# Kernel optimization log

Hardware: AMD Instinct MI355X
Metric: run time of the kernel (lower is better)

Reference implementation:

```python
import jax, jax.numpy as jnp
import numpy as np

ALPHA = 0.5      # APPNP teleport prob (AG_EAGCN alpha=0.5)
DEPTH = 3        # APPNP depth
PROP_NUMS = 3    # EAGCN propagation steps


def _adj_process(adj, eps):
    # adj[adj<eps]=0 ; symmetrize ; add I ; D^-1/2 A D^-1/2 (inf->0)
    N = adj.shape[1]
    adj = jnp.where(adj < eps, 0.0, adj)
    adj = 0.5 * (adj + jnp.swapaxes(adj, 1, 2))
    adj = adj + jnp.eye(N, dtype=adj.dtype)
    d = jnp.sum(adj, axis=2)                                   # [n, N]
    dinv = jnp.where(d > 0, 1.0 / jnp.sqrt(jnp.where(d > 0, d, 1.0)), 0.0)
    return adj * dinv[:, :, None] * dinv[:, None, :]


def _eagcn(seg, edge, ws1, bs1, ws11, bs11, ws2, bs2, ws3, bs3, wmlp, bmlp, wgcn, bgcn):
    n, c, h, w = seg.shape
    hw = h * w
    num_s = ws1.shape[0]
    # conv_s1 (1x1)
    seg_s = jnp.einsum('nchw,sc->nshw', seg, ws1) + bs1[None, :, None, None]
    theta_T = seg_s.reshape(n, num_s, hw)       # raw view, as in torch
    theta = seg_s.reshape(n, hw, num_s)         # raw view (NOT transpose)
    # channel attention: diag_channel_att = ca ca^T is rank-1 ->
    # theta @ (ca ca^T) @ theta_T = (theta@ca) outer (ca@theta_T)
    pooled = seg.mean(axis=(2, 3))                              # [n, c]
    ca = jax.nn.relu(pooled @ wmlp.T + bmlp)                    # [n, num_s]
    u = jnp.einsum('nps,ns->np', theta, ca)                     # [n, hw]
    v = jnp.einsum('ns,nsq->nq', ca, theta_T)                   # [n, hw]
    sim_c = _adj_process(u[:, :, None] * v[:, None, :], 0.15)
    # spatial branch
    seg_c = jnp.einsum('nchw,sc->nshw', seg, ws11) + bs11[None, :, None, None]
    sigma = seg_c.reshape(n, num_s, hw)
    sigma_T = seg_c.reshape(n, hw, num_s)
    sigma_out = jnp.einsum('nps,nsq->npq', sigma_T, sigma)      # [n, hw, hw]
    edge_m = seg * edge
    seg_ss = (ws2 * seg.max(axis=1) + bs2).reshape(n, 1, hw)    # 1x1 conv on 1 chan
    edge_mm = (ws3 * edge_m.max(axis=1) + bs3).reshape(n, hw, 1)
    sim_s = _adj_process(sigma_out * (edge_mm * seg_ss), 0.15)
    sim = _adj_process(sim_c + sim_s, 0.0)
    # GCN_layer: relu(conv1d(seg @ sim)) + seg, residual
    seg2 = seg.reshape(n, c, hw)
    seg_sim = jnp.einsum('nck,nkq->ncq', seg2, sim)
    out = jax.nn.relu(jnp.einsum('oc,ncq->noq', wgcn, seg_sim) + bgcn[None, :, None]) + seg2
    return out.reshape(n, c, h, w), sim


def _appnp(seg, adj, wa1, ba1, wa2, ba2):
    n, c, h, w = seg.shape
    x = seg.reshape(n, h * w, c)                                # raw view
    t = jax.nn.relu(jax.nn.relu(x @ wa1.T + ba1) @ wa2.T + ba2)
    out = t
    for _ in range(DEPTH):
        out = (1.0 - ALPHA) * jnp.einsum('npq,nqc->npc', adj, out) + ALPHA * t
    return out


def _forward(seg, edge, ws1, bs1, ws11, bs11, ws2, bs2, ws3, bs3,
             wmlp, bmlp, wgcn, bgcn, wa1, ba1, wa2, ba2):
    ori = seg
    n, c, h, w = seg.shape
    adjs = []
    for _ in range(PROP_NUMS):
        seg, adj = _eagcn(seg, edge, ws1, bs1, ws11, bs11, ws2, bs2, ws3, bs3,
                          wmlp, bmlp, wgcn, bgcn)
        adjs.append(adj)
    adj = (adjs[0] + adjs[1] + adjs[2]) / float(PROP_NUMS)      # mean aggregation
    adj = _adj_process(adj, 0.0)
    # graph regularizer
    dirichlet = jnp.einsum('nii->', adj)                        # sum of traces
    N = adj.shape[1]
    gamma = 0.1; beta = 0.1; alpha_r = 0.1
    rowsum = jnp.sum(adj, axis=2)                               # adj @ ones
    f_A = (-beta * jnp.sum(jnp.log(rowsum), axis=1)[:, None, None] / N
           + gamma * jnp.sqrt(jnp.sum(adj * adj)) / (N ** 2))
    reg = alpha_r * dirichlet + f_A                             # [n,1,1]
    out = _appnp(ori, adj, wa1, ba1, wa2, ba2).reshape(n, c, h, w)
    return out, reg


def setup_inputs() -> dict:
    key = jax.random.key(0)
    ks = jax.random.split(key, 10)
    n, c, h, w = 8, 256, 32, 32
    num_s, hid = 64, 3

    def lin(k, out_f, in_f):
        lim = 1.0 / np.sqrt(in_f)
        return jax.random.uniform(k, (out_f, in_f), jnp.float32, -lim, lim)

    return dict(
        seg=jax.random.normal(ks[0], (n, c, h, w), jnp.float32),
        edge=jax.random.uniform(ks[1], (n, c, h, w), jnp.float32),
        ws1=lin(ks[2], num_s, c), bs1=jnp.zeros((num_s,), jnp.float32),
        ws11=lin(ks[3], num_s, c), bs11=jnp.zeros((num_s,), jnp.float32),
        ws2=jnp.asarray(0.7, jnp.float32), bs2=jnp.asarray(0.1, jnp.float32),
        ws3=jnp.asarray(0.6, jnp.float32), bs3=jnp.asarray(0.1, jnp.float32),
        wmlp=lin(ks[4], num_s, c), bmlp=jnp.zeros((num_s,), jnp.float32),
        wgcn=lin(ks[5], c, c), bgcn=jnp.zeros((c,), jnp.float32),
        wa1=lin(ks[6], hid, c), ba1=jnp.zeros((hid,), jnp.float32),
        wa2=lin(ks[7], c, hid), ba2=jnp.zeros((c,), jnp.float32),
    )


def reference(seg, edge, ws1, bs1, ws11, bs11, ws2, bs2, ws3, bs3,
              wmlp, bmlp, wgcn, bgcn, wa1, ba1, wa2, ba2):
    return _forward(seg, edge, ws1, bs1, ws11, bs11, ws2, bs2, ws3, bs3,
                    wmlp, bmlp, wgcn, bgcn, wa1, ba1, wa2, ba2)
```

## Files before the change

kernel.cpp:

```cpp
#include <hip/hip_runtime.h>
#include <math.h>

#define NB 8
#define C 256
#define HW 1024
#define NS 64

typedef unsigned short u16;
typedef __attribute__((ext_vector_type(8))) short bf16x8;
typedef __attribute__((ext_vector_type(4))) float f32x4;

__device__ __forceinline__ u16 f2bf(float x) {
    union { float f; unsigned u; } v; v.f = x;
    unsigned r = v.u + 0x7fffu + ((v.u >> 16) & 1u);
    return (u16)(r >> 16);
}
__device__ __forceinline__ float bf2f(u16 h) {
    union { unsigned u; float f; } v; v.u = ((unsigned)h) << 16; return v.f;
}
__device__ __forceinline__ void splitbf(float x, u16& h, u16& l) {
    h = f2bf(x);
    l = f2bf(x - bf2f(h));
}

__device__ __forceinline__ float blockReduceSum(float v, float* s4) {
    #pragma unroll
    for (int o = 32; o; o >>= 1) v += __shfl_down(v, o);
    __syncthreads();
    if ((threadIdx.x & 63) == 0) s4[threadIdx.x >> 6] = v;
    __syncthreads();
    return s4[0] + s4[1] + s4[2] + s4[3];
}

__global__ void k_presplit(const float* __restrict__ in, u16* __restrict__ oh,
                           u16* __restrict__ ol, int nElem) {
    for (int i = blockIdx.x * 256 + threadIdx.x; i < nElem; i += gridDim.x * 256) {
        u16 h, l; splitbf(in[i], h, l);
        oh[i] = h; ol[i] = l;
    }
}

__global__ void k_prepw(const float* __restrict__ ws1, const float* __restrict__ bs1,
                        const float* __restrict__ ws11, const float* __restrict__ bs11,
                        u16* __restrict__ WCH, u16* __restrict__ WCL, float* __restrict__ BCAT) {
    int tid = blockIdx.x * 256 + threadIdx.x;
    if (tid < 64 * C) {
        u16 h, l;
        splitbf(ws1[tid], h, l);  WCH[tid] = h;          WCL[tid] = l;
        splitbf(ws11[tid], h, l); WCH[64 * C + tid] = h; WCL[64 * C + tid] = l;
    }
    if (tid < 64) { BCAT[tid] = bs1[tid]; BCAT[64 + tid] = bs11[tid]; }
}

template<int R, int CIN, bool WF32>
__global__ void k_transp_split(const float* __restrict__ in, long long sIn,
                               u16* __restrict__ oh, u16* __restrict__ ol,
                               float* __restrict__ of, long long sOut) {
    int ti = blockIdx.x, tj = blockIdx.y, n = blockIdx.z, tid = threadIdx.x;
    int i0 = ti * 64, j0 = tj * 64;
    const float* ib = in + (size_t)n * sIn;
    __shared__ float L[64][65];
    for (int idx = tid; idx < 4096; idx += 256) {
        int r = idx >> 6, c = idx & 63;
        L[r][c] = ib[(size_t)(i0 + r) * CIN + (j0 + c)];
    }
    __syncthreads();
    for (int idx = tid; idx < 4096; idx += 256) {
        int r = idx >> 6, c = idx & 63;
        size_t o = (size_t)n * sOut + (size_t)(j0 + r) * R + (i0 + c);
        float val = L[c][r];
        u16 h, l; splitbf(val, h, l);
        oh[o] = h; ol[o] = l;
        if (WF32) of[o] = val;
    }
}

__global__ void k_pooled(const float* __restrict__ seg, float* __restrict__ pooled) {
    int c = blockIdx.x, n = blockIdx.y, tid = threadIdx.x;
    const float* row = seg + ((size_t)n * C + c) * HW;
    float acc = row[tid] + row[tid + 256] + row[tid + 512] + row[tid + 768];
    __shared__ float s4[4];
    float r = blockReduceSum(acc, s4);
    if (tid == 0) pooled[n * C + c] = r * (1.0f / HW);
}

__global__ void k_ca(const float* __restrict__ pooled, const float* __restrict__ wmlp,
                     const float* __restrict__ bmlp, float* __restrict__ ca) {
    int n = blockIdx.x, s = threadIdx.x;
    __shared__ float pl[C];
    for (int i = s; i < C; i += 64) pl[i] = pooled[n * C + i];
    __syncthreads();
    float acc = 0.f;
    for (int c = 0; c < C; ++c) acc += pl[c] * wmlp[s * C + c];
    float r = acc + bmlp[s];
    ca[n * NS + s] = r > 0.f ? r : 0.f;
}

__global__ void k_maxes(const float* __restrict__ seg, const float* __restrict__ edge,
                        float* __restrict__ smax, float* __restrict__ emax) {
    int pos = blockIdx.x * 256 + threadIdx.x;
    int n = blockIdx.y, ch = blockIdx.z;
    const float* sb = seg + (size_t)n * C * HW + (size_t)(ch * 32) * HW + pos;
    const float* eb = edge + (size_t)n * C * HW + (size_t)(ch * 32) * HW + pos;
    float ms = -3.402823466e38f, me = -3.402823466e38f;
    #pragma unroll 8
    for (int c = 0; c < 32; ++c) {
        float s = sb[(size_t)c * HW];
        ms = fmaxf(ms, s);
        me = fmaxf(me, s * eb[(size_t)c * HW]);
    }
    smax[((size_t)ch * NB + n) * HW + pos] = ms;
    emax[((size_t)ch * NB + n) * HW + pos] = me;
}

__global__ void k_maxfin(const float* __restrict__ smax, const float* __restrict__ emax,
                         const float* __restrict__ ws2, const float* __restrict__ bs2,
                         const float* __restrict__ ws3, const float* __restrict__ bs3,
                         float* __restrict__ segss, float* __restrict__ edgemm,
                         float* __restrict__ dsum) {
    int pos = blockIdx.x * 256 + threadIdx.x;
    int n = blockIdx.y;
    float ms = -3.402823466e38f, me = -3.402823466e38f;
    #pragma unroll
    for (int ch = 0; ch < 8; ++ch) {
        ms = fmaxf(ms, smax[((size_t)ch * NB + n) * HW + pos]);
        me = fmaxf(me, emax[((size_t)ch * NB + n) * HW + pos]);
    }
    segss[n * HW + pos] = ws2[0] * ms + bs2[0];
    edgemm[n * HW + pos] = ws3[0] * me + bs3[0];
    dsum[n * HW + pos] = 0.f;
}

__global__ void k_uv(const float* __restrict__ segsc, const float* __restrict__ ca,
                     float* __restrict__ u, float* __restrict__ vv) {
    int pos = blockIdx.x * 256 + threadIdx.x;
    int n = blockIdx.y, role = blockIdx.z;
    const float* flat = segsc + (size_t)n * 128 * HW;
    __shared__ float cs[NS];
    if (threadIdx.x < NS) cs[threadIdx.x] = ca[n * NS + threadIdx.x];
    __syncthreads();
    if (role == 0) {
        const float* base = flat + (size_t)pos * NS;
        float acc = 0.f;
        #pragma unroll
        for (int s = 0; s < NS; ++s) acc += base[s] * cs[s];
        u[n * HW + pos] = acc;
    } else {
        float acc = 0.f;
        #pragma unroll
        for (int s = 0; s < NS; ++s) acc += cs[s] * flat[(size_t)s * HW + pos];
        vv[n * HW + pos] = acc;
    }
}

__global__ __launch_bounds__(256) void k_bbuild(
    const u16* __restrict__ AH, const u16* __restrict__ AL, long long sA,
    const u16* __restrict__ CTH, const u16* __restrict__ CTL, long long sCT,
    const float* __restrict__ em, const float* __restrict__ ss,
    float* __restrict__ B, float* __restrict__ dsum) {
    constexpr int LDK = 72;
    constexpr int TSZ = 64 * LDK;
    __shared__ __align__(16) u16 sm[4 * 2 * TSZ];
    int pi = blockIdx.x, n = blockIdx.y, tid = threadIdx.x;
    int i = 0, base = 0;
    while (pi >= base + (16 - i)) { base += 16 - i; ++i; }
    int j = i + (pi - base);
    int i0 = i * 64, j0 = j * 64;
    bool diag = (i == j);
    const u16* AnH = AH + (size_t)n * sA;
    const u16* AnL = AL + (size_t)n * sA;
    const u16* CnH = CTH + (size_t)n * sCT;
    const u16* CnL = CTL + (size_t)n * sCT;
    const float* emn = em + n * HW;
    const float* ssn = ss + n * HW;
    float* Bn = B + (size_t)n * HW * HW;

    auto stage = [&](int t, const u16* srcH, const u16* srcL, int r0) {
        u16* hi = sm + t * 2 * TSZ;
        u16* lo = hi + TSZ;
        #pragma unroll
        for (int p = 0; p < 2; ++p) {
            int e = (p * 256 + tid) * 8;
            int r = e >> 6, k0 = e & 63;
            size_t off = (size_t)(r0 + r) * 64 + k0;
            int b = r * LDK + k0;
            *(bf16x8*)(hi + b) = *(const bf16x8*)(srcH + off);
            *(bf16x8*)(lo + b) = *(const bf16x8*)(srcL + off);
        }
    };
    stage(0, AnH, AnL, i0);
    stage(2, CnH, CnL, i0);
    if (!diag) { stage(1, AnH, AnL, j0); stage(3, CnH, CnL, j0); }
    __syncthreads();

    int lane = tid & 63, wv = tid >> 6;
    int g = lane >> 4;
    f32x4 acc1[4], acc2[4];
    #pragma unroll
    for (int ni = 0; ni < 4; ++ni) {
        acc1[ni] = (f32x4){0.f, 0.f, 0.f, 0.f};
        acc2[ni] = (f32x4){0.f, 0.f, 0.f, 0.f};
    }

    const u16* AiH = sm + 0 * 2 * TSZ; const u16* AiL = AiH + TSZ;
    const u16* AjH = sm + 1 * 2 * TSZ; const u16* AjL = AjH + TSZ;
    const u16* BiH = sm + 2 * 2 * TSZ; const u16* BiL = BiH + TSZ;
    const u16* BjH = sm + 3 * 2 * TSZ; const u16* BjL = BjH + TSZ;

    #pragma unroll
    for (int kk = 0; kk < 2; ++kk) {
        int kl = kk * 32 + g * 8;
        int arow = wv * 16 + (lane & 15);
        bf16x8 a1h = *(const bf16x8*)(AiH + arow * LDK + kl);
        bf16x8 a1l = *(const bf16x8*)(AiL + arow * LDK + kl);
        bf16x8 a2h, a2l;
        if (!diag) {
            a2h = *(const bf16x8*)(AjH + arow * LDK + kl);
            a2l = *(const bf16x8*)(AjL + arow * LDK + kl);
        }
        #pragma unroll
        for (int ni = 0; ni < 4; ++ni) {
            int brow = ni * 16 + (lane & 15);
            if (diag) {
                bf16x8 bh = *(const bf16x8*)(BiH + brow * LDK + kl);
                bf16x8 bl = *(const bf16x8*)(BiL + brow * LDK + kl);
                acc1[ni] = __builtin_amdgcn_mfma_f32_16x16x32_bf16(a1h, bh, acc1[ni], 0, 0, 0);
                acc1[ni] = __builtin_amdgcn_mfma_f32_16x16x32_bf16(a1h, bl, acc1[ni], 0, 0, 0);
                acc1[ni] = __builtin_amdgcn_mfma_f32_16x16x32_bf16(a1l, bh, acc1[ni], 0, 0, 0);
            } else {
                bf16x8 b1h = *(const bf16x8*)(BjH + brow * LDK + kl);
                bf16x8 b1l = *(const bf16x8*)(BjL + brow * LDK + kl);
                acc1[ni] = __builtin_amdgcn_mfma_f32_16x16x32_bf16(a1h, b1h, acc1[ni], 0, 0, 0);
                acc1[ni] = __builtin_amdgcn_mfma_f32_16x16x32_bf16(a1h, b1l, acc1[ni], 0, 0, 0);
                acc1[ni] = __builtin_amdgcn_mfma_f32_16x16x32_bf16(a1l, b1h, acc1[ni], 0, 0, 0);
                bf16x8 b2h = *(const bf16x8*)(BiH + brow * LDK + kl);
                bf16x8 b2l = *(const bf16x8*)(BiL + brow * LDK + kl);
                acc2[ni] = __builtin_amdgcn_mfma_f32_16x16x32_bf16(a2h, b2h, acc2[ni], 0, 0, 0);
                acc2[ni] = __builtin_amdgcn_mfma_f32_16x16x32_bf16(a2h, b2l, acc2[ni], 0, 0, 0);
                acc2[ni] = __builtin_amdgcn_mfma_f32_16x16x32_bf16(a2l, b2h, acc2[ni], 0, 0, 0);
            }
        }
    }
    __syncthreads();

    float* t1 = (float*)sm;
    float* t2 = t1 + 64 * 65;
    float x[4][4], y[4][4];
    #pragma unroll
    for (int ni = 0; ni < 4; ++ni) {
        int col = ni * 16 + (lane & 15);
        #pragma unroll
        for (int r = 0; r < 4; ++r) {
            int row = wv * 16 + g * 4 + r;
            float v1 = acc1[ni][r] * emn[i0 + row] * ssn[j0 + col];
            v1 = v1 < 0.15f ? 0.f : v1;
            x[ni][r] = v1;
            t1[row * 65 + col] = v1;
            if (!diag) {
                float v2 = acc2[ni][r] * emn[j0 + row] * ssn[i0 + col];
                v2 = v2 < 0.15f ? 0.f : v2;
                y[ni][r] = v2;
                t2[row * 65 + col] = v2;
            }
        }
    }
    __syncthreads();

    float rs1[4] = {0.f, 0.f, 0.f, 0.f}, rs2[4] = {0.f, 0.f, 0.f, 0.f};
    #pragma unroll
    for (int ni = 0; ni < 4; ++ni) {
        int col = ni * 16 + (lane & 15);
        #pragma unroll
        for (int r = 0; r < 4; ++r) {
            int row = wv * 16 + g * 4 + r;
            float s1 = 0.5f * (x[ni][r] + (diag ? t1[col * 65 + row] : t2[col * 65 + row]));
            Bn[(size_t)(i0 + row) * HW + j0 + col] = s1;
            rs1[r] += s1;
            if (!diag) {
                float s2 = 0.5f * (y[ni][r] + t1[col * 65 + row]);
                Bn[(size_t)(j0 + row) * HW + i0 + col] = s2;
                rs2[r] += s2;
            }
        }
    }
    #pragma unroll
    for (int r = 0; r < 4; ++r) {
        #pragma unroll
        for (int m = 1; m < 16; m <<= 1) {
            rs1[r] += __shfl_xor(rs1[r], m);
            rs2[r] += __shfl_xor(rs2[r], m);
        }
    }
    if ((lane & 15) == 0) {
        #pragma unroll
        for (int r = 0; r < 4; ++r) {
            int row = wv * 16 + g * 4 + r;
            atomicAdd(&dsum[n * HW + i0 + row], rs1[r]);
            if (!diag) atomicAdd(&dsum[n * HW + j0 + row], rs2[r]);
        }
    }
}

template<int BM, int BN, int MODE>
__global__ __launch_bounds__(256) void k_mfma3(
    const u16* __restrict__ AH, const u16* __restrict__ AL, long long sA, int lda,
    const u16* __restrict__ BH, const u16* __restrict__ BL, long long sB, int ldb,
    int K,
    float* __restrict__ Cf, u16* __restrict__ CH, u16* __restrict__ CL,
    long long sC, int ldc,
    const float* __restrict__ e1,
    const float* __restrict__ e2, long long se2) {
    constexpr int WM = BM / 32;
    constexpr int WN = BN / 32;
    constexpr int LDK = 72;
    __shared__ __align__(16) u16 smem[(BM + BN) * LDK * 2];
    u16* sAH = smem;
    u16* sAL = smem + BM * LDK;
    u16* sBH = smem + 2 * BM * LDK;
    u16* sBL = smem + 2 * BM * LDK + BN * LDK;
    int n = blockIdx.z;
    int q0 = blockIdx.x * BN, m0 = blockIdx.y * BM;
    int tid = threadIdx.x, lane = tid & 63, wv = tid >> 6;
    int wm = wv >> 1, wn = wv & 1;

    f32x4 acc[WM][WN];
    #pragma unroll
    for (int mi = 0; mi < WM; ++mi)
        #pragma unroll
        for (int ni = 0; ni < WN; ++ni)
            acc[mi][ni] = (f32x4){0.f, 0.f, 0.f, 0.f};

    for (int kt = 0; kt < K; kt += 64) {
        #pragma unroll
        for (int p = 0; p < BM / 32; ++p) {
            int e = (p * 256 + tid) * 8;
            int r = e >> 6, k0 = e & 63;
            size_t off = (size_t)n * sA + (size_t)(m0 + r) * lda + kt + k0;
            int b = r * LDK + k0;
            *(bf16x8*)(sAH + b) = *(const bf16x8*)(AH + off);
            *(bf16x8*)(sAL + b) = *(const bf16x8*)(AL + off);
        }
        #pragma unroll
        for (int p = 0; p < BN / 32; ++p) {
            int e = (p * 256 + tid) * 8;
            int c = e >> 6, k0 = e & 63;
            size_t off = (size_t)n * sB + (size_t)(q0 + c) * ldb + kt + k0;
            int b = c * LDK + k0;
            *(bf16x8*)(sBH + b) = *(const bf16x8*)(BH + off);
            *(bf16x8*)(sBL + b) = *(const bf16x8*)(BL + off);
        }
        __syncthreads();
        #pragma unroll
        for (int kk = 0; kk < 2; ++kk) {
            int klocal = kk * 32 + (lane >> 4) * 8;
            bf16x8 aH[WM], aL[WM], bH[WN], bL[WN];
            #pragma unroll
            for (int mi = 0; mi < WM; ++mi) {
                int row = (wm * WM + mi) * 16 + (lane & 15);
                aH[mi] = *(const bf16x8*)(sAH + row * LDK + klocal);
                aL[mi] = *(const bf16x8*)(sAL + row * LDK + klocal);
            }
            #pragma unroll
            for (int ni = 0; ni < WN; ++ni) {
                int col = (wn * WN + ni) * 16 + (lane & 15);
                bH[ni] = *(const bf16x8*)(sBH + col * LDK + klocal);
                bL[ni] = *(const bf16x8*)(sBL + col * LDK + klocal);
            }
            #pragma unroll
            for (int mi = 0; mi < WM; ++mi)
                #pragma unroll
                for (int ni = 0; ni < WN; ++ni) {
                    acc[mi][ni] = __builtin_amdgcn_mfma_f32_16x16x32_bf16(aH[mi], bH[ni], acc[mi][ni], 0, 0, 0);
                    acc[mi][ni] = __builtin_amdgcn_mfma_f32_16x16x32_bf16(aH[mi], bL[ni], acc[mi][ni], 0, 0, 0);
                    acc[mi][ni] = __builtin_amdgcn_mfma_f32_16x16x32_bf16(aL[mi], bH[ni], acc[mi][ni], 0, 0, 0);
                }
        }
        __syncthreads();
    }

    if (MODE == 0) {
        u16* Th = smem;
        u16* Tl = smem + BN * (BM + 1);
        #pragma unroll
        for (int mi = 0; mi < WM; ++mi) {
            #pragma unroll
            for (int ni = 0; ni < WN; ++ni) {
                int cl = (wn * WN + ni) * 16 + (lane & 15);
                int rb = (wm * WM + mi) * 16 + (lane >> 4) * 4;
                #pragma unroll
                for (int r = 0; r < 4; ++r) {
                    u16 h, l; splitbf(acc[mi][ni][r], h, l);
                    Th[cl * (BM + 1) + rb + r] = h;
                    Tl[cl * (BM + 1) + rb + r] = l;
                }
            }
        }
        __syncthreads();
        for (int idx = tid; idx < BM * BN; idx += 256) {
            int q = idx / BM, m = idx % BM;
            size_t o = (size_t)n * sC + (size_t)(q0 + q) * ldc + (m0 + m);
            CH[o] = Th[q * (BM + 1) + m];
            CL[o] = Tl[q * (BM + 1) + m];
        }
    } else if (MODE == 4) {
        float* Tf = (float*)smem;
        #pragma unroll
        for (int mi = 0; mi < WM; ++mi) {
            #pragma unroll
            for (int ni = 0; ni < WN; ++ni) {
                int cl = (wn * WN + ni) * 16 + (lane & 15);
                int rb = (wm * WM + mi) * 16 + (lane >> 4) * 4;
                #pragma unroll
                for (int r = 0; r < 4; ++r) {
                    int row = m0 + rb + r, col = q0 + cl;
                    float val = 0.5f * acc[mi][ni][r]
                              + 0.5f * e2[(size_t)n * se2 + (size_t)row * HW + col];
                    Tf[cl * (BM + 1) + rb + r] = val;
                }
            }
        }
        __syncthreads();
        for (int idx = tid; idx < BM * BN; idx += 256) {
            int q = idx / BM, m = idx % BM;
            Cf[(size_t)n * sC + (size_t)(q0 + q) * ldc + (m0 + m)] = Tf[q * (BM + 1) + m];
        }
    } else {
        #pragma unroll
        for (int mi = 0; mi < WM; ++mi) {
            #pragma unroll
            for (int ni = 0; ni < WN; ++ni) {
                int col = q0 + (wn * WN + ni) * 16 + (lane & 15);
                int rowb = m0 + (wm * WM + mi) * 16 + (lane >> 4) * 4;
                #pragma unroll
                for (int r = 0; r < 4; ++r) {
                    int row = rowb + r;
                    float val = acc[mi][ni][r];
                    if (MODE == 2) {
                        val = fmaxf(val + e1[row], 0.f) + e2[(size_t)n * se2 + (size_t)row * ldc + col];
                        size_t o = (size_t)n * sC + (size_t)row * ldc + col;
                        Cf[o] = val;
                        u16 h, l; splitbf(val, h, l);
                        CH[o] = h; CL[o] = l;
                    } else if (MODE == 3) {
                        val = 0.5f * val + 0.5f * e2[(size_t)n * se2 + (size_t)row * ldc + col];
                        size_t o = (size_t)n * sC + (size_t)row * ldc + col;
                        u16 h, l; splitbf(val, h, l);
                        CH[o] = h; CL[o] = l;
                    } else {
                        val = val + e1[row];
                        size_t o = (size_t)n * sC + (size_t)row * ldc + col;
                        Cf[o] = val;
                        u16 h, l; splitbf(val, h, l);
                        CH[o] = h; CL[o] = l;
                    }
                }
            }
        }
    }
}

__global__ void k_dinv(const float* __restrict__ u, const float* __restrict__ vv,
                       const float* __restrict__ dsum,
                       float* __restrict__ dcinv, float* __restrict__ dsinv) {
    int p = blockIdx.x, n = blockIdx.y, tid = threadIdx.x;
    const float* un = u + n * HW;
    const float* vn = vv + n * HW;
    float up = un[p], vp = vn[p];
    float acc_c = 0.f;
    for (int q = tid; q < HW; q += 256) {
        float x = up * vn[q]; x = x < 0.15f ? 0.f : x;
        float y = un[q] * vp; y = y < 0.15f ? 0.f : y;
        acc_c += 0.5f * (x + y);
    }
    __shared__ float s4[4];
    acc_c = blockReduceSum(acc_c, s4);
    if (tid == 0) {
        dcinv[n * HW + p] = 1.0f / sqrtf(acc_c + 1.0f);
        dsinv[n * HW + p] = 1.0f / sqrtf(dsum[n * HW + p] + 1.0f);
    }
}

__global__ void k_simsum(const float* __restrict__ B, const float* __restrict__ u,
                         const float* __restrict__ vv, const float* __restrict__ dcinv,
                         const float* __restrict__ dsinv, float* __restrict__ dfinv) {
    int p = blockIdx.x, n = blockIdx.y, tid = threadIdx.x;
    const float* Bb = B + (size_t)n * HW * HW + (size_t)p * HW;
    const float* un = u + n * HW;
    const float* vn = vv + n * HW;
    const float* dci = dcinv + n * HW;
    const float* dsi = dsinv + n * HW;
    float up = un[p], vp = vn[p], dcp = dci[p], dsp = dsi[p];
    float acc = 0.f;
    for (int q = tid; q < HW; q += 256) {
        float x = up * vn[q]; x = x < 0.15f ? 0.f : x;
        float y = un[q] * vp; y = y < 0.15f ? 0.f : y;
        float delta = (q == p) ? 1.0f : 0.0f;
        float val = (0.5f * (x + y) + delta) * dcp * dci[q] + (Bb[q] + delta) * dsp * dsi[q];
        acc += val;
    }
    __shared__ float s4[4];
    acc = blockReduceSum(acc, s4);
    if (tid == 0) dfinv[n * HW + p] = 1.0f / sqrtf(acc + 1.0f);
}

__global__ void k_norm_accum(const float* __restrict__ B, const float* __restrict__ u,
                             const float* __restrict__ vv, const float* __restrict__ dcinv,
                             const float* __restrict__ dsinv, const float* __restrict__ dfinv,
                             u16* __restrict__ SMH, u16* __restrict__ SML,
                             float* __restrict__ ACC, int first) {
    int p = blockIdx.x, n = blockIdx.y, tid = threadIdx.x;
    const float* Bb = B + (size_t)n * HW * HW + (size_t)p * HW;
    u16* Sh = SMH + (size_t)n * HW * HW + (size_t)p * HW;
    u16* Sl = SML + (size_t)n * HW * HW + (size_t)p * HW;
    float* Ab = ACC + (size_t)n * HW * HW + (size_t)p * HW;
    const float* un = u + n * HW;
    const float* vn = vv + n * HW;
    const float* dci = dcinv + n * HW;
    const float* dsi = dsinv + n * HW;
    const float* df = dfinv + n * HW;
    float up = un[p], vp = vn[p], dcp = dci[p], dsp = dsi[p], dfp = df[p];
    for (int q = tid; q < HW; q += 256) {
        float x = up * vn[q]; x = x < 0.15f ? 0.f : x;
        float y = un[q] * vp; y = y < 0.15f ? 0.f : y;
        float delta = (q == p) ? 1.0f : 0.0f;
        float sim_pre = (0.5f * (x + y) + delta) * dcp * dci[q] + (Bb[q] + delta) * dsp * dsi[q];
        float val = (sim_pre + delta) * dfp * df[q];
        u16 h, l; splitbf(val, h, l);
        Sh[q] = h; Sl[q] = l;
        Ab[q] = first ? val : (Ab[q] + val);
    }
}

__global__ void k_final_rowsum(const float* __restrict__ ACC, float* __restrict__ dinv) {
    int p = blockIdx.x, n = blockIdx.y, tid = threadIdx.x;
    const float* Ab = ACC + (size_t)n * HW * HW + (size_t)p * HW;
    float acc = 0.f;
    for (int q = tid; q < HW; q += 256) acc += Ab[q];
    __shared__ float s4[4];
    acc = blockReduceSum(acc, s4);
    if (tid == 0) dinv[n * HW + p] = 1.0f / sqrtf(acc * (1.0f / 3.0f) + 1.0f);
}

__global__ void k_final_norm(const float* __restrict__ ACC, const float* __restrict__ dinv,
                             u16* __restrict__ ADJH, u16* __restrict__ ADJL,
                             float* __restrict__ rowsf, float* __restrict__ diagrow,
                             float* __restrict__ sqrow) {
    int p = blockIdx.x, n = blockIdx.y, tid = threadIdx.x;
    const float* Ab = ACC + (size_t)n * HW * HW + (size_t)p * HW;
    u16* Oh = ADJH + (size_t)n * HW * HW + (size_t)p * HW;
    u16* Ol = ADJL + (size_t)n * HW * HW + (size_t)p * HW;
    const float* di = dinv + n * HW;
    float dp = di[p];
    float accr = 0.f, accsq = 0.f, accd = 0.f;
    for (int q = tid; q < HW; q += 256) {
        float val = (Ab[q] * (1.0f / 3.0f) + ((q == p) ? 1.f : 0.f)) * dp * di[q];
        u16 h, l; splitbf(val, h, l);
        Oh[q] = h; Ol[q] = l;
        accr += val;
        accsq += val * val;
        if (q == p) accd = val;
    }
    __shared__ float s4[4];
    accr = blockReduceSum(accr, s4);
    accsq = blockReduceSum(accsq, s4);
    accd = blockReduceSum(accd, s4);
    if (tid == 0) {
        rowsf[n * HW + p] = accr;
        sqrow[n * HW + p] = accsq;
        diagrow[n * HW + p] = accd;
    }
}

__global__ void k_reg(const float* __restrict__ rowsf, const float* __restrict__ diagrow,
                      const float* __restrict__ sqrow, float* __restrict__ outreg) {
    int n = blockIdx.x, tid = threadIdx.x;
    float acc = 0.f, a = 0.f, b = 0.f;
    for (int p = tid; p < HW; p += 256) acc += logf(rowsf[n * HW + p]);
    for (int i = tid; i < NB * HW; i += 256) { a += diagrow[i]; b += sqrow[i]; }
    __shared__ float s4[4];
    acc = blockReduceSum(acc, s4);
    a = blockReduceSum(a, s4);
    b = blockReduceSum(b, s4);
    if (tid == 0) {
        float f = -0.1f * acc / 1024.0f + 0.1f * sqrtf(b) / 1048576.0f;
        outreg[n] = 0.1f * a + f;
    }
}

__global__ void k_appnp_t(const float* __restrict__ ori, const float* __restrict__ wa1,
                          const float* __restrict__ ba1, const float* __restrict__ wa2,
                          const float* __restrict__ ba2, float* __restrict__ T) {
    int p = blockIdx.x, n = blockIdx.y, tid = threadIdx.x;
    const float* x = ori + (size_t)n * C * HW + (size_t)p * C;
    float xv = x[tid];
    __shared__ float s4[4];
    __shared__ float h[3];
    float d0 = blockReduceSum(xv * wa1[0 * C + tid], s4);
    float d1 = blockReduceSum(xv * wa1[1 * C + tid], s4);
    float d2 = blockReduceSum(xv * wa1[2 * C + tid], s4);
    if (tid == 0) {
        h[0] = fmaxf(d0 + ba1[0], 0.f);
        h[1] = fmaxf(d1 + ba1[1], 0.f);
        h[2] = fmaxf(d2 + ba1[2], 0.f);
    }
    __syncthreads();
    float t = h[0] * wa2[tid * 3 + 0] + h[1] * wa2[tid * 3 + 1] + h[2] * wa2[tid * 3 + 2] + ba2[tid];
    T[(size_t)n * HW * C + (size_t)p * C + tid] = fmaxf(t, 0.f);
}

extern "C" void kernel_launch(void* const* d_in, const int* in_sizes, int n_in,
                              void* d_out, int out_size, void* d_ws, size_t ws_size,
                              hipStream_t stream) {
    const float* seg_in = (const float*)d_in[0];
    const float* edge   = (const float*)d_in[1];
    const float* ws1    = (const float*)d_in[2];
    const float* bs1    = (const float*)d_in[3];
    const float* ws11   = (const float*)d_in[4];
    const float* bs11   = (const float*)d_in[5];
    const float* ws2    = (const float*)d_in[6];
    const float* bs2    = (const float*)d_in[7];
    const float* ws3    = (const float*)d_in[8];
    const float* bs3    = (const float*)d_in[9];
    const float* wmlp   = (const float*)d_in[10];
    const float* bmlp   = (const float*)d_in[11];
    const float* wgcn   = (const float*)d_in[12];
    const float* bgcn   = (const float*)d_in[13];
    const float* wa1    = (const float*)d_in[14];
    const float* ba1    = (const float*)d_in[15];
    const float* wa2    = (const float*)d_in[16];
    const float* ba2    = (const float*)d_in[17];

    float* out = (float*)d_out;
    char* wb = (char*)d_ws;
    size_t off = 0;
    auto nf = [&](size_t elems) -> float* {
        float* p = (float*)(wb + off); off += ((elems * 4 + 255) & ~(size_t)255); return p; };
    auto nu = [&](size_t elems) -> u16* {
        u16* p = (u16*)(wb + off); off += ((elems * 2 + 255) & ~(size_t)255); return p; };

    float* SEG_A   = nf((size_t)NB * C * HW);
    float* SEGSC   = nf((size_t)NB * 128 * HW);
    float* TT      = nf((size_t)NB * C * HW);
    float* TBUF    = nf((size_t)NB * HW * C);
    float* BBUF    = nf((size_t)NB * HW * HW);
    float* ACCUM   = nf((size_t)NB * HW * HW);
    float* MAXS    = nf((size_t)8 * NB * HW);
    float* MAXE    = nf((size_t)8 * NB * HW);
    float* BCAT    = nf(128);
    float* ubuf    = nf(NB * HW);
    float* vbuf    = nf(NB * HW);
    float* ssbuf   = nf(NB * HW);
    float* embuf   = nf(NB * HW);
    float* dsum    = nf(NB * HW);
    float* dcinv   = nf(NB * HW);
    float* dsinv   = nf(NB * HW);
    float* dfinv   = nf(NB * HW);
    float* rowsf   = nf(NB * HW);
    float* diagrow = nf(NB * HW);
    float* sqrow   = nf(NB * HW);
    float* pooled  = nf(NB * C);
    float* cabuf   = nf(NB * NS);
    float* scal    = nf(16);
    u16* SAH  = nu((size_t)NB * C * HW);   u16* SAL  = nu((size_t)NB * C * HW);
    u16* TGH  = nu((size_t)NB * HW * C);   u16* TGL  = nu((size_t)NB * HW * C);
    u16* WCH  = nu((size_t)128 * C);       u16* WCL  = nu((size_t)128 * C);
    u16* WGH  = nu((size_t)C * C);         u16* WGL  = nu((size_t)C * C);
    u16* SCH  = nu((size_t)NB * 128 * HW); u16* SCL  = nu((size_t)NB * 128 * HW);
    u16* CTH  = nu((size_t)NB * HW * NS);  u16* CTL  = nu((size_t)NB * HW * NS);
    u16* SMH  = nu((size_t)NB * HW * HW);  u16* SML  = nu((size_t)NB * HW * HW);
    u16* SIMTH= nu((size_t)NB * HW * C);   u16* SIMTL= nu((size_t)NB * HW * C);
    u16* TTH  = nu((size_t)NB * C * HW);   u16* TTL  = nu((size_t)NB * C * HW);
    u16* X1H  = nu((size_t)NB * C * HW);   u16* X1L  = nu((size_t)NB * C * HW);
    u16* X2H  = nu((size_t)NB * C * HW);   u16* X2L  = nu((size_t)NB * C * HW);
    u16* ADJH = SMH;
    u16* ADJL = SML;
    (void)scal;

    const long long sAdj = (long long)HW * HW;
    const long long sSeg = (long long)C * HW;
    const long long sSC  = (long long)128 * HW;
    const long long sCT  = (long long)HW * NS;

    k_prepw<<<dim3(64), 256, 0, stream>>>(ws1, bs1, ws11, bs11, WCH, WCL, BCAT);
    k_presplit<<<dim3(64), 256, 0, stream>>>(wgcn, WGH, WGL, C * C);
    k_presplit<<<dim3(2048), 256, 0, stream>>>(seg_in, SAH, SAL, NB * C * HW);

    for (int it = 0; it < 3; ++it) {
        const float* seg_src = (it == 0) ? seg_in : SEG_A;
        k_transp_split<C, HW, false><<<dim3(4, 16, NB), 256, 0, stream>>>(
            seg_src, sSeg, TGH, TGL, nullptr, sSeg);
        k_mfma3<32, 64, 5><<<dim3(16, 4, NB), 256, 0, stream>>>(
            WCH, WCL, 0, C, TGH, TGL, sSeg, C, C,
            SEGSC, SCH, SCL, sSC, HW, BCAT, nullptr, 0);
        k_transp_split<NS, HW, false><<<dim3(1, 16, NB), 256, 0, stream>>>(
            SEGSC + (size_t)64 * HW, sSC, CTH, CTL, nullptr, sCT);
        k_pooled<<<dim3(C, NB), 256, 0, stream>>>(seg_src, pooled);
        k_ca<<<dim3(NB), 64, 0, stream>>>(pooled, wmlp, bmlp, cabuf);
        k_maxes<<<dim3(4, NB, 8), 256, 0, stream>>>(seg_src, edge, MAXS, MAXE);
        k_maxfin<<<dim3(4, NB), 256, 0, stream>>>(MAXS, MAXE, ws2, bs2, ws3, bs3,
                                                  ssbuf, embuf, dsum);
        k_uv<<<dim3(4, NB, 2), 256, 0, stream>>>(SEGSC, cabuf, ubuf, vbuf);
        k_bbuild<<<dim3(136, NB), 256, 0, stream>>>(
            SCH + (size_t)64 * HW, SCL + (size_t)64 * HW, sSC,
            CTH, CTL, sCT, embuf, ssbuf, BBUF, dsum);
        k_dinv<<<dim3(HW, NB), 256, 0, stream>>>(ubuf, vbuf, dsum, dcinv, dsinv);
        k_simsum<<<dim3(HW, NB), 256, 0, stream>>>(BBUF, ubuf, vbuf, dcinv, dsinv, dfinv);
        k_norm_accum<<<dim3(HW, NB), 256, 0, stream>>>(BBUF, ubuf, vbuf, dcinv, dsinv, dfinv,
                                                       SMH, SML, ACCUM, it == 0 ? 1 : 0);
        k_mfma3<32, 64, 0><<<dim3(16, 8, NB), 256, 0, stream>>>(
            SAH, SAL, sSeg, HW, SMH, SML, sAdj, HW, HW,
            nullptr, SIMTH, SIMTL, sSeg, C, nullptr, nullptr, 0);
        k_mfma3<32, 64, 2><<<dim3(16, 8, NB), 256, 0, stream>>>(
            WGH, WGL, 0, C, SIMTH, SIMTL, sSeg, C, C,
            SEG_A, SAH, SAL, sSeg, HW, bgcn, seg_src, sSeg);
    }

    k_final_rowsum<<<dim3(HW, NB), 256, 0, stream>>>(ACCUM, dcinv);
    k_final_norm<<<dim3(HW, NB), 256, 0, stream>>>(ACCUM, dcinv, ADJH, ADJL, rowsf, diagrow, sqrow);
    k_reg<<<dim3(NB), 256, 0, stream>>>(rowsf, diagrow, sqrow, out + (size_t)NB * C * HW);

    k_appnp_t<<<dim3(HW, NB), 256, 0, stream>>>(seg_in, wa1, ba1, wa2, ba2, TBUF);
    k_transp_split<HW, C, true><<<dim3(16, 4, NB), 256, 0, stream>>>(
        TBUF, sSeg, TTH, TTL, TT, sSeg);
    k_mfma3<32, 64, 3><<<dim3(16, 8, NB), 256, 0, stream>>>(
        TTH, TTL, sSeg, HW, ADJH, ADJL, sAdj, HW, HW,
        nullptr, X1H, X1L, sSeg, HW, nullptr, TT, sSeg);
    k_mfma3<32, 64, 3><<<dim3(16, 8, NB), 256, 0, stream>>>(
        X1H, X1L, sSeg, HW, ADJH, ADJL, sAdj, HW, HW,
        nullptr, X2H, X2L, sSeg, HW, nullptr, TT, sSeg);
    k_mfma3<32, 64, 4><<<dim3(16, 8, NB), 256, 0, stream>>>(
        X2H, X2L, sSeg, HW, ADJH, ADJL, sAdj, HW, HW,
        out, nullptr, nullptr, sSeg, C, nullptr, TT, sSeg);
}
```

Measured before the change: 606.1 us.

## Store pre-normalized sim in place, fuse final rowsum, enlarge MFMA tiles

k_simsum now writes the combined pre-normalization similarity back into BBUF, so k_norm_accum only rescales it instead of recomputing the u/v thresholding and both normalizations. k_norm_accum also accumulates row sums of the accumulated adjacency, which removes the separate full pass over ACCUM in k_final_rowsum and leaves a tiny elementwise kernel. Separately, all MFMA GEMM launches switch from 32x64 to 64x64 tiles with half the blocks in M. The tile change raises per-block reuse but lowers block count and may raise register pressure.

```diff
diff --git a/kernel.cpp b/kernel.cpp
--- a/kernel.cpp
+++ b/kernel.cpp
@@ -480,11 +480,11 @@
     }
 }
 
-__global__ void k_simsum(const float* __restrict__ B, const float* __restrict__ u,
-                         const float* __restrict__ vv, const float* __restrict__ dcinv,
-                         const float* __restrict__ dsinv, float* __restrict__ dfinv) {
+__global__ void k_build_sim(float* __restrict__ B, const float* __restrict__ u,
+                            const float* __restrict__ vv, const float* __restrict__ dcinv,
+                            const float* __restrict__ dsinv, float* __restrict__ dfinv) {
     int p = blockIdx.x, n = blockIdx.y, tid = threadIdx.x;
-    const float* Bb = B + (size_t)n * HW * HW + (size_t)p * HW;
+    float* Bb = B + (size_t)n * HW * HW + (size_t)p * HW;
     const float* un = u + n * HW;
     const float* vn = vv + n * HW;
     const float* dci = dcinv + n * HW;
@@ -496,6 +496,7 @@
         float y = un[q] * vp; y = y < 0.15f ? 0.f : y;
         float delta = (q == p) ? 1.0f : 0.0f;
         float val = (0.5f * (x + y) + delta) * dcp * dci[q] + (Bb[q] + delta) * dsp * dsi[q];
+        Bb[q] = val;
         acc += val;
     }
     __shared__ float s4[4];
@@ -503,42 +504,32 @@
     if (tid == 0) dfinv[n * HW + p] = 1.0f / sqrtf(acc + 1.0f);
 }
 
-__global__ void k_norm_accum(const float* __restrict__ B, const float* __restrict__ u,
-                             const float* __restrict__ vv, const float* __restrict__ dcinv,
-                             const float* __restrict__ dsinv, const float* __restrict__ dfinv,
+__global__ void k_norm_accum(const float* __restrict__ B, const float* __restrict__ dfinv,
                              u16* __restrict__ SMH, u16* __restrict__ SML,
-                             float* __restrict__ ACC, int first) {
+                             float* __restrict__ ACC, float* __restrict__ rowacc, int first) {
     int p = blockIdx.x, n = blockIdx.y, tid = threadIdx.x;
     const float* Bb = B + (size_t)n * HW * HW + (size_t)p * HW;
     u16* Sh = SMH + (size_t)n * HW * HW + (size_t)p * HW;
     u16* Sl = SML + (size_t)n * HW * HW + (size_t)p * HW;
     float* Ab = ACC + (size_t)n * HW * HW + (size_t)p * HW;
-    const float* un = u + n * HW;
-    const float* vn = vv + n * HW;
-    const float* dci = dcinv + n * HW;
-    const float* dsi = dsinv + n * HW;
     const float* df = dfinv + n * HW;
-    float up = un[p], vp = vn[p], dcp = dci[p], dsp = dsi[p], dfp = df[p];
+    float dfp = df[p];
+    float racc = 0.f;
     for (int q = tid; q < HW; q += 256) {
-        float x = up * vn[q]; x = x < 0.15f ? 0.f : x;
-        float y = un[q] * vp; y = y < 0.15f ? 0.f : y;
-        float delta = (q == p) ? 1.0f : 0.0f;
-        float sim_pre = (0.5f * (x + y) + delta) * dcp * dci[q] + (Bb[q] + delta) * dsp * dsi[q];
-        float val = (sim_pre + delta) * dfp * df[q];
+        float val = (Bb[q] + ((q == p) ? 1.f : 0.f)) * dfp * df[q];
         u16 h, l; splitbf(val, h, l);
         Sh[q] = h; Sl[q] = l;
         Ab[q] = first ? val : (Ab[q] + val);
-    }
-}
-
-__global__ void k_final_rowsum(const float* __restrict__ ACC, float* __restrict__ dinv) {
-    int p = blockIdx.x, n = blockIdx.y, tid = threadIdx.x;
-    const float* Ab = ACC + (size_t)n * HW * HW + (size_t)p * HW;
-    float acc = 0.f;
-    for (int q = tid; q < HW; q += 256) acc += Ab[q];
+        racc += val;
+    }
     __shared__ float s4[4];
-    acc = blockReduceSum(acc, s4);
-    if (tid == 0) dinv[n * HW + p] = 1.0f / sqrtf(acc * (1.0f / 3.0f) + 1.0f);
+    racc = blockReduceSum(racc, s4);
+    if (tid == 0) rowacc[n * HW + p] = first ? racc : (rowacc[n * HW + p] + racc);
+}
+
+__global__ void k_dinvfin(const float* __restrict__ rowacc, float* __restrict__ dinv) {
+    int i = blockIdx.x * 256 + threadIdx.x;
+    if (i < NB * HW) dinv[i] = 1.0f / sqrtf(rowacc[i] * (1.0f / 3.0f) + 1.0f);
 }
 
 __global__ void k_final_norm(const float* __restrict__ ACC, const float* __restrict__ dinv,
@@ -655,12 +646,12 @@
     float* dcinv   = nf(NB * HW);
     float* dsinv   = nf(NB * HW);
     float* dfinv   = nf(NB * HW);
+    float* rowacc  = nf(NB * HW);
     float* rowsf   = nf(NB * HW);
     float* diagrow = nf(NB * HW);
     float* sqrow   = nf(NB * HW);
     float* pooled  = nf(NB * C);
     float* cabuf   = nf(NB * NS);
-    float* scal    = nf(16);
     u16* SAH  = nu((size_t)NB * C * HW);   u16* SAL  = nu((size_t)NB * C * HW);
     u16* TGH  = nu((size_t)NB * HW * C);   u16* TGL  = nu((size_t)NB * HW * C);
     u16* WCH  = nu((size_t)128 * C);       u16* WCL  = nu((size_t)128 * C);
@@ -674,7 +665,6 @@
     u16* X2H  = nu((size_t)NB * C * HW);   u16* X2L  = nu((size_t)NB * C * HW);
     u16* ADJH = SMH;
     u16* ADJL = SML;
-    (void)scal;
 
     const long long sAdj = (long long)HW * HW;
     const long long sSeg = (long long)C * HW;
@@ -689,7 +679,7 @@
         const float* seg_src = (it == 0) ? seg_in : SEG_A;
         k_transp_split<C, HW, false><<<dim3(4, 16, NB), 256, 0, stream>>>(
             seg_src, sSeg, TGH, TGL, nullptr, sSeg);
-        k_mfma3<32, 64, 5><<<dim3(16, 4, NB), 256, 0, stream>>>(
+        k_mfma3<64, 64, 5><<<dim3(16, 2, NB), 256, 0, stream>>>(
             WCH, WCL, 0, C, TGH, TGL, sSeg, C, C,
             SEGSC, SCH, SCL, sSC, HW, BCAT, nullptr, 0);
         k_transp_split<NS, HW, false><<<dim3(1, 16, NB), 256, 0, stream>>>(
@@ -704,31 +694,31 @@
             SCH + (size_t)64 * HW, SCL + (size_t)64 * HW, sSC,
             CTH, CTL, sCT, embuf, ssbuf, BBUF, dsum);
         k_dinv<<<dim3(HW, NB), 256, 0, stream>>>(ubuf, vbuf, dsum, dcinv, dsinv);
-        k_simsum<<<dim3(HW, NB), 256, 0, stream>>>(BBUF, ubuf, vbuf, dcinv, dsinv, dfinv);
-        k_norm_accum<<<dim3(HW, NB), 256, 0, stream>>>(BBUF, ubuf, vbuf, dcinv, dsinv, dfinv,
-                                                       SMH, SML, ACCUM, it == 0 ? 1 : 0);
-        k_mfma3<32, 64, 0><<<dim3(16, 8, NB), 256, 0, stream>>>(
+        k_build_sim<<<dim3(HW, NB), 256, 0, stream>>>(BBUF, ubuf, vbuf, dcinv, dsinv, dfinv);
+        k_norm_accum<<<dim3(HW, NB), 256, 0, stream>>>(BBUF, dfinv, SMH, SML, ACCUM, rowacc,
+                                                       it == 0 ? 1 : 0);
+        k_mfma3<64, 64, 0><<<dim3(16, 4, NB), 256, 0, stream>>>(
             SAH, SAL, sSeg, HW, SMH, SML, sAdj, HW, HW,
             nullptr, SIMTH, SIMTL, sSeg, C, nullptr, nullptr, 0);
-        k_mfma3<32, 64, 2><<<dim3(16, 8, NB), 256, 0, stream>>>(
+        k_mfma3<64, 64, 2><<<dim3(16, 4, NB), 256, 0, stream>>>(
             WGH, WGL, 0, C, SIMTH, SIMTL, sSeg, C, C,
             SEG_A, SAH, SAL, sSeg, HW, bgcn, seg_src, sSeg);
     }
 
-    k_final_rowsum<<<dim3(HW, NB), 256, 0, stream>>>(ACCUM, dcinv);
+    k_dinvfin<<<dim3(32), 256, 0, stream>>>(rowacc, dcinv);
     k_final_norm<<<dim3(HW, NB), 256, 0, stream>>>(ACCUM, dcinv, ADJH, ADJL, rowsf, diagrow, sqrow);
     k_reg<<<dim3(NB), 256, 0, stream>>>(rowsf, diagrow, sqrow, out + (size_t)NB * C * HW);
 
     k_appnp_t<<<dim3(HW, NB), 256, 0, stream>>>(seg_in, wa1, ba1, wa2, ba2, TBUF);
     k_transp_split<HW, C, true><<<dim3(16, 4, NB), 256, 0, stream>>>(
         TBUF, sSeg, TTH, TTL, TT, sSeg);
-    k_mfma3<32, 64, 3><<<dim3(16, 8, NB), 256, 0, stream>>>(
+    k_mfma3<64, 64, 3><<<dim3(16, 4, NB), 256, 0, stream>>>(
         TTH, TTL, sSeg, HW, ADJH, ADJL, sAdj, HW, HW,
         nullptr, X1H, X1L, sSeg, HW, nullptr, TT, sSeg);
-    k_mfma3<32, 64, 3><<<dim3(16, 8, NB), 256, 0, stream>>>(
+    k_mfma3<64, 64, 3><<<dim3(16, 4, NB), 256, 0, stream>>>(
         X1H, X1L, sSeg, HW, ADJH, ADJL, sAdj, HW, HW,
         nullptr, X2H, X2L, sSeg, HW, nullptr, TT, sSeg);
-    k_mfma3<32, 64, 4><<<dim3(16, 8, NB), 256, 0, stream>>>(
+    k_mfma3<64, 64, 4><<<dim3(16, 4, NB), 256, 0, stream>>>(
         X2H, X2L, sSeg, HW, ADJH, ADJL, sAdj, HW, HW,
         out, nullptr, nullptr, sSeg, C, nullptr, TT, sSeg);
 }
```

Result: faster. 584.8 us (median of 2 runs) (-3.5%).
